# Kernel optimization log

Measured on AMD Instinct MI355X. Metric: run time of the kernel, lower is better.

## Reference

```python
import jax, jax.numpy as jnp
import numpy as np

B, S, D, H, L, FF = 1, 2048, 512, 8, 4, 2048
DH = D // H


def _sincos(n, d):
    theta = 1.0 / (10000.0 ** (np.arange(0, d, 2, dtype=np.float64) / d))
    ang = np.arange(n, dtype=np.float64)[:, None] * theta[None, :]
    sin = np.repeat(np.sin(ang), 2, axis=-1).astype(np.float32)
    cos = np.repeat(np.cos(ang), 2, axis=-1).astype(np.float32)
    return jnp.asarray(sin), jnp.asarray(cos)  # [n, d]


def _rot(x):
    # rotate pairs: (x1, x2) -> (-x2, x1), interleaved
    x1, x2 = x[..., 0::2], x[..., 1::2]
    return jnp.stack([-x2, x1], axis=-1).reshape(x.shape)


def _theta_shift(x, sin, cos):
    return x * cos + _rot(x) * sin


def _decay_mask(n, h):
    # RetNet per-head decay gammas: 1 - exp(linspace(log(1/32), log(1/512), h))
    gammas = 1.0 - np.exp(np.linspace(np.log(1.0 / 32.0), np.log(1.0 / 512.0), h))
    dist = np.arange(n)[:, None] - np.arange(n)[None, :]
    m = np.where(dist >= 0, gammas[:, None, None] ** np.maximum(dist, 0), 0.0)
    return jnp.asarray(m, dtype=jnp.float32)  # [h, n, n]


def _ln(x, w, b, eps=1e-5):
    mu = x.mean(-1, keepdims=True)
    var = ((x - mu) ** 2).mean(-1, keepdims=True)
    return (x - mu) * jax.lax.rsqrt(var + eps) * w + b


def setup_inputs() -> dict:
    key = jax.random.key(0)
    ks = jax.random.split(key, 12)
    sc = 0.02
    nrm = lambda k, shp: jax.random.normal(k, shp, jnp.float32) * sc
    return {
        "x": jax.random.normal(ks[0], (B, S, D), jnp.float32),
        "pos_emb": nrm(ks[1], (5000, D)),
        "Wq": nrm(ks[2], (L, D, D)), "bq": jnp.zeros((L, D), jnp.float32),
        "Wk": nrm(ks[3], (L, D, D)), "bk": jnp.zeros((L, D), jnp.float32),
        "Wv": nrm(ks[4], (L, D, D)), "bv": jnp.zeros((L, D), jnp.float32),
        "Wg": nrm(ks[5], (L, D, D)), "bg": jnp.zeros((L, D), jnp.float32),
        "Wo": nrm(ks[6], (L, D, D)), "bo": jnp.zeros((L, D), jnp.float32),
        "ln1w": jnp.ones((L, D), jnp.float32), "ln1b": jnp.zeros((L, D), jnp.float32),
        "ln2w": jnp.ones((L, D), jnp.float32), "ln2b": jnp.zeros((L, D), jnp.float32),
        "W1": nrm(ks[7], (L, D, FF)), "b1": jnp.zeros((L, FF), jnp.float32),
        "W2": nrm(ks[8], (L, FF, D)), "b2": jnp.zeros((L, D), jnp.float32),
        "Wout": nrm(ks[9], (D, 1)), "bout": jnp.zeros((1,), jnp.float32),
    }


def reference(x, pos_emb, Wq, bq, Wk, bk, Wv, bv, Wg, bg, Wo, bo,
              ln1w, ln1b, ln2w, ln2b, W1, b1, W2, b2, Wout, bout):
    b, s, d = x.shape
    # faithful to source: pos_emb[:x.shape[0]] (requires B==1 to broadcast)
    x = x + pos_emb[: x.shape[0]]
    sin, cos = _sincos(s, DH)
    dmask = _decay_mask(s, H)  # [h, s, s]
    inv_scale = 1.0 / jnp.sqrt(jnp.float32(DH))

    def heads(t):  # [b,s,d] -> [b,h,s,dh]
        return t.reshape(b, s, H, DH).transpose(0, 2, 1, 3)

    for l in range(L):
        # --- multi-scale retention block (pre-LN) ---
        y = _ln(x, ln1w[l], ln1b[l])
        q = heads(y @ Wq[l] + bq[l])
        k = heads(y @ Wk[l] + bk[l])
        v = heads(y @ Wv[l] + bv[l])
        q = _theta_shift(q, sin, cos) * inv_scale
        k = _theta_shift(k, sin, cos)
        sim = jnp.einsum("bhnd,bhmd->bhnm", q, k) * dmask  # decay-masked QK^T
        ret = jnp.einsum("bhnm,bhmd->bhnd", sim, v)
        # per-head group norm (no affine)
        mu = ret.mean(-1, keepdims=True)
        var = ((ret - mu) ** 2).mean(-1, keepdims=True)
        ret = (ret - mu) * jax.lax.rsqrt(var + 1e-6)
        ret = ret.transpose(0, 2, 1, 3).reshape(b, s, d)
        g = jax.nn.silu(y @ Wg[l] + bg[l])
        x = x + (g * ret) @ Wo[l] + bo[l]
        # --- FFN block (pre-LN, swish) ---
        z = _ln(x, ln2w[l], ln2b[l])
        x = x + jax.nn.silu(z @ W1[l] + b1[l]) @ W2[l] + b2[l]

    return jax.nn.sigmoid(x @ Wout + bout)  # [b, s, 1]
```

## Files before the change

kernel.cpp:

```cpp
#include <hip/hip_runtime.h>
#include <math.h>
#include <stdint.h>

#define SEQ 2048
#define DMODEL 512
#define NH 8
#define DHEAD 64
#define NL 4
#define DFF 2048

typedef __attribute__((ext_vector_type(8))) short short8;
typedef __attribute__((ext_vector_type(4))) float f32x4;

__device__ __forceinline__ short f2bf(float f) {
  unsigned u = __float_as_uint(f);
  u += 0x7fffu + ((u >> 16) & 1u);
  return (short)(u >> 16);
}
__device__ __forceinline__ float silu_f(float x) { return x / (1.f + __expf(-x)); }

__device__ __forceinline__ void cp16(const void* g, void* l) {
  __builtin_amdgcn_global_load_lds(
      (const __attribute__((address_space(1))) unsigned*)(unsigned long long)(uintptr_t)g,
      (__attribute__((address_space(3))) unsigned*)(unsigned)(uintptr_t)l, 16, 0, 0);
}

__global__ __launch_bounds__(256) void k_transpose(const float* __restrict__ src, short* __restrict__ dst,
                                                   int rows, int cols) {
  __shared__ float tile[32][33];
  size_t zoff = (size_t)blockIdx.z * rows * cols;
  src += zoff; dst += zoff;
  int bx = blockIdx.x * 32, by = blockIdx.y * 32;
  int tx = threadIdx.x & 31, ty = threadIdx.x >> 5;
#pragma unroll
  for (int k = 0; k < 4; ++k)
    tile[ty + k * 8][tx] = src[(size_t)(by + ty + k * 8) * cols + bx + tx];
  __syncthreads();
#pragma unroll
  for (int k = 0; k < 4; ++k)
    dst[(size_t)(bx + ty + k * 8) * rows + by + tx] = f2bf(tile[tx][ty + k * 8]);
}

__global__ void k_addpos(const float* __restrict__ xi, const float* __restrict__ pos, float* __restrict__ xo) {
  int i = blockIdx.x * 256 + threadIdx.x;
  float4 a = ((const float4*)xi)[i];
  float4 p = ((const float4*)pos)[i & 127];
  a.x += p.x; a.y += p.y; a.z += p.z; a.w += p.w;
  ((float4*)xo)[i] = a;
}

__global__ void k_sincos(float* __restrict__ sn, float* __restrict__ cs) {
  int g = blockIdx.x * 256 + threadIdx.x;
  int s = g >> 5, p = g & 31;
  double inv = pow(10000.0, -(double)p / 32.0);
  double a = (double)s * inv;
  float sv = (float)sin(a), cv = (float)cos(a);
  sn[s * DHEAD + 2 * p] = sv; sn[s * DHEAD + 2 * p + 1] = sv;
  cs[s * DHEAD + 2 * p] = cv; cs[s * DHEAD + 2 * p + 1] = cv;
}

__global__ __launch_bounds__(256) void k_ln(const float* __restrict__ x, const float* __restrict__ w,
                                            const float* __restrict__ b, short* __restrict__ o, float eps) {
  int wid = threadIdx.x >> 6, lane = threadIdx.x & 63;
  int row = blockIdx.x * 4 + wid;
  const float* xr = x + (size_t)row * DMODEL;
  float4 v0 = *(const float4*)(xr + lane * 8);
  float4 v1 = *(const float4*)(xr + lane * 8 + 4);
  float sm = v0.x + v0.y + v0.z + v0.w + v1.x + v1.y + v1.z + v1.w;
  float sq = v0.x * v0.x + v0.y * v0.y + v0.z * v0.z + v0.w * v0.w +
             v1.x * v1.x + v1.y * v1.y + v1.z * v1.z + v1.w * v1.w;
#pragma unroll
  for (int m = 1; m < 64; m <<= 1) { sm += __shfl_xor(sm, m); sq += __shfl_xor(sq, m); }
  float mu = sm * (1.f / 512.f);
  float rstd = rsqrtf(sq * (1.f / 512.f) - mu * mu + eps);
  const float* wr = w + lane * 8; const float* br = b + lane * 8;
  float vals[8] = {v0.x, v0.y, v0.z, v0.w, v1.x, v1.y, v1.z, v1.w};
  short t[8] __attribute__((aligned(16)));
#pragma unroll
  for (int i = 0; i < 8; ++i) t[i] = f2bf((vals[i] - mu) * rstd * wr[i] + br[i]);
  *(int4*)(o + (size_t)row * DMODEL + lane * 8) = *(int4*)t;
}

struct GB { const short* A; const short* Bt; const float* bias; void* out; int mode; };
struct GArgs { GB b[4]; int M, N, K; };

__global__ __launch_bounds__(256) void k_gemm(GArgs ga) {
  const GB g = ga.b[blockIdx.z];
  const int K = ga.K, N = ga.N, M = ga.M;
  const int n0 = blockIdx.x * 64;
  const int m0 = blockIdx.y * 64;
  const int tid = threadIdx.x;
  const int w = tid >> 6, lane = tid & 63, l16 = lane & 15, quad = lane >> 4;
  const int wm = (w & 1) * 32, wn = (w >> 1) * 32;
  __shared__ __align__(16) short As[2][4096];
  __shared__ __align__(16) short Bs[2][4096];

  const short* Ab = g.A + (size_t)m0 * K;
  const short* Bb = g.Bt + (size_t)n0 * K;
  const int rsub = lane >> 3;
  const int cch = (lane & 7) ^ rsub;
  const int nIter = K >> 6;

  auto stage = [&](int buf, int k0) {
#pragma unroll
    for (int c = 0; c < 2; ++c) {
      int seg = w + 4 * c;
      cp16(Ab + (size_t)(seg * 8 + rsub) * K + k0 + cch * 8, &As[buf][seg * 512]);
      cp16(Bb + (size_t)(seg * 8 + rsub) * K + k0 + cch * 8, &Bs[buf][seg * 512]);
    }
  };

  f32x4 acc[2][2];
#pragma unroll
  for (int a = 0; a < 2; ++a)
#pragma unroll
    for (int b = 0; b < 2; ++b) acc[a][b] = {0.f, 0.f, 0.f, 0.f};

  stage(0, 0);
  for (int it = 0; it < nIter; ++it) {
    __syncthreads();
    if (it + 1 < nIter) stage((it + 1) & 1, (it + 1) << 6);
    const short* as = As[it & 1];
    const short* bs = Bs[it & 1];
#pragma unroll
    for (int kki = 0; kki < 2; ++kki) {
      int ch = ((quad + 4 * kki) ^ (l16 & 7)) * 8;
      short8 af[2], bfv[2];
#pragma unroll
      for (int a = 0; a < 2; ++a) af[a] = *(const short8*)&as[(wm + a * 16 + l16) * 64 + ch];
#pragma unroll
      for (int b = 0; b < 2; ++b) bfv[b] = *(const short8*)&bs[(wn + b * 16 + l16) * 64 + ch];
#pragma unroll
      for (int a = 0; a < 2; ++a)
#pragma unroll
        for (int b = 0; b < 2; ++b)
          acc[a][b] = __builtin_amdgcn_mfma_f32_16x16x32_bf16(af[a], bfv[b], acc[a][b], 0, 0, 0);
    }
  }
#pragma unroll
  for (int a = 0; a < 2; ++a) {
#pragma unroll
    for (int b = 0; b < 2; ++b) {
      int row0 = m0 + wm + a * 16 + quad * 4;
      int col = n0 + wn + b * 16 + l16;
      float vals[4];
#pragma unroll
      for (int r = 0; r < 4; ++r) vals[r] = acc[a][b][r] + g.bias[col];
      if (g.mode == 4) {
        short t4[4] __attribute__((aligned(8)));
#pragma unroll
        for (int r = 0; r < 4; ++r) t4[r] = f2bf(vals[r]);
        *(uint2*)&((short*)g.out)[(size_t)col * M + row0] = *(const uint2*)t4;
      } else if (g.mode == 0) {
#pragma unroll
        for (int r = 0; r < 4; ++r) ((float*)g.out)[(size_t)(row0 + r) * N + col] = vals[r];
      } else if (g.mode == 1) {
#pragma unroll
        for (int r = 0; r < 4; ++r) ((short*)g.out)[(size_t)(row0 + r) * N + col] = f2bf(silu_f(vals[r]));
      } else {
#pragma unroll
        for (int r = 0; r < 4; ++r) ((float*)g.out)[(size_t)(row0 + r) * N + col] += vals[r];
      }
    }
  }
}

__global__ __launch_bounds__(256) void k_rope(const float* __restrict__ q, const float* __restrict__ k,
                                              const float* __restrict__ sn, const float* __restrict__ cs,
                                              short* __restrict__ qo, short* __restrict__ ko) {
  int s = blockIdx.x * 2 + (threadIdx.x >> 7);
  int idx = (threadIdx.x & 127) * 4;
  int d = idx & 63;
  size_t base = (size_t)s * DMODEL + idx;
  float4 qv = *(const float4*)(q + base);
  float4 kv = *(const float4*)(k + base);
  float4 sv = *(const float4*)(sn + s * DHEAD + d);
  float4 cv = *(const float4*)(cs + s * DHEAD + d);
  short qt[4] __attribute__((aligned(8))), kt[4] __attribute__((aligned(8)));
  qt[0] = f2bf((qv.x * cv.x - qv.y * sv.x) * 0.125f);
  qt[1] = f2bf((qv.y * cv.y + qv.x * sv.y) * 0.125f);
  qt[2] = f2bf((qv.z * cv.z - qv.w * sv.z) * 0.125f);
  qt[3] = f2bf((qv.w * cv.w + qv.z * sv.w) * 0.125f);
  kt[0] = f2bf(kv.x * cv.x - kv.y * sv.x);
  kt[1] = f2bf(kv.y * cv.y + kv.x * sv.y);
  kt[2] = f2bf(kv.z * cv.z - kv.w * sv.z);
  kt[3] = f2bf(kv.w * cv.w + kv.z * sv.w);
  *(uint2*)(qo + base) = *(const uint2*)qt;
  *(uint2*)(ko + base) = *(const uint2*)kt;
}

__global__ __launch_bounds__(256) void k_attn(const short* __restrict__ qb, const short* __restrict__ kb,
                                              const short* __restrict__ vtb, float* __restrict__ r0,
                                              float* __restrict__ r1) {
  int x = blockIdx.x, hd = blockIdx.y, jc = blockIdx.z;
  int ib = jc ? (31 - x) : x;
  int t = threadIdx.x;
  int w = t >> 6, lane = t & 63, l16 = lane & 15, quad = lane >> 4;
  __shared__ __align__(16) short smem[4 * 64 * 72];
  short* qs = smem;
  short* kt = smem + 4608;
  short* vt = smem + 9216;
  short* p  = smem + 13824;

  double stepd = (log(1.0 / 512.0) - log(1.0 / 32.0)) / 7.0;
  double gam = 1.0 - exp(log(1.0 / 32.0) + hd * stepd);
  float l2g = (float)(log(gam) * 1.4426950408889634);

  for (int c = t; c < 512; c += 256) {
    int r = c >> 3, d8 = (c & 7) * 8;
    *(short8*)&qs[r * 72 + d8] = *(const short8*)&qb[(size_t)(ib * 64 + r) * DMODEL + hd * DHEAD + d8];
  }
  f32x4 oacc[4];
#pragma unroll
  for (int b = 0; b < 4; ++b) oacc[b] = {0.f, 0.f, 0.f, 0.f};

  for (int jb = jc; jb <= ib; jb += 2) {
    __syncthreads();
    for (int c = t; c < 512; c += 256) {
      int r = c >> 3, d8 = (c & 7) * 8;
      *(short8*)&kt[r * 72 + d8] = *(const short8*)&kb[(size_t)(jb * 64 + r) * DMODEL + hd * DHEAD + d8];
      *(short8*)&vt[r * 72 + d8] = *(const short8*)&vtb[(size_t)(hd * DHEAD + r) * SEQ + jb * 64 + d8];
    }
    __syncthreads();
    f32x4 sacc[4];
#pragma unroll
    for (int b = 0; b < 4; ++b) sacc[b] = {0.f, 0.f, 0.f, 0.f};
#pragma unroll
    for (int kk = 0; kk < 64; kk += 32) {
      short8 af = *(const short8*)&qs[(w * 16 + l16) * 72 + kk + quad * 8];
#pragma unroll
      for (int b = 0; b < 4; ++b) {
        short8 bf_ = *(const short8*)&kt[(b * 16 + l16) * 72 + kk + quad * 8];
        sacc[b] = __builtin_amdgcn_mfma_f32_16x16x32_bf16(af, bf_, sacc[b], 0, 0, 0);
      }
    }
    int dtile = (ib - jb) * 64;
#pragma unroll
    for (int b = 0; b < 4; ++b) {
#pragma unroll
      for (int r = 0; r < 4; ++r) {
        int iloc = w * 16 + quad * 4 + r;
        int jloc = b * 16 + l16;
        int df = dtile + iloc - jloc;
        float dec = (df < 0) ? 0.f : exp2f(l2g * (float)df);
        p[iloc * 72 + jloc] = f2bf(sacc[b][r] * dec);
      }
    }
    __syncthreads();
#pragma unroll
    for (int kk = 0; kk < 64; kk += 32) {
      short8 af = *(const short8*)&vt[(w * 16 + l16) * 72 + kk + quad * 8];
#pragma unroll
      for (int b = 0; b < 4; ++b) {
        short8 bf_ = *(const short8*)&p[(b * 16 + l16) * 72 + kk + quad * 8];
        oacc[b] = __builtin_amdgcn_mfma_f32_16x16x32_bf16(af, bf_, oacc[b], 0, 0, 0);
      }
    }
  }
  __syncthreads();
  float* obuf = (float*)smem;
#pragma unroll
  for (int b = 0; b < 4; ++b) {
#pragma unroll
    for (int r = 0; r < 4; ++r) {
      int d = w * 16 + quad * 4 + r;
      int i = b * 16 + l16;
      obuf[i * 68 + d] = oacc[b][r];
    }
  }
  __syncthreads();
  float* rp = jc ? r1 : r0;
  for (int c = t; c < 1024; c += 256) {
    int r = c >> 4, d4 = (c & 15) * 4;
    *(float4*)&rp[(size_t)(ib * 64 + r) * DMODEL + hd * DHEAD + d4] = *(const float4*)&obuf[r * 68 + d4];
  }
}

__global__ __launch_bounds__(256) void k_retgate(const float* __restrict__ r0, const float* __restrict__ r1,
                                                 const float* __restrict__ g, short* __restrict__ o) {
  int wid = threadIdx.x >> 6, lane = threadIdx.x & 63;
  int row = blockIdx.x * 4 + wid;
  int s = row >> 3, hd = row & 7;
  size_t base = (size_t)s * DMODEL + hd * DHEAD + lane;
  float v = r0[base] + r1[base];
  float sm = v, sq = v * v;
#pragma unroll
  for (int m = 1; m < 64; m <<= 1) { sm += __shfl_xor(sm, m); sq += __shfl_xor(sq, m); }
  float mu = sm * (1.f / 64.f);
  float var = sq * (1.f / 64.f) - mu * mu;
  float rn = (v - mu) * rsqrtf(var + 1e-6f);
  o[base] = f2bf(silu_f(g[base]) * rn);
}

__global__ __launch_bounds__(256) void k_final(const float* __restrict__ x, const float* __restrict__ w,
                                               const float* __restrict__ bo, float* __restrict__ o) {
  int wid = threadIdx.x >> 6, lane = threadIdx.x & 63;
  int row = blockIdx.x * 4 + wid;
  const float* xr = x + (size_t)row * DMODEL;
  float4 a0 = *(const float4*)(xr + lane * 8), a1 = *(const float4*)(xr + lane * 8 + 4);
  float4 w0 = *(const float4*)(w + lane * 8), w1 = *(const float4*)(w + lane * 8 + 4);
  float sm = a0.x * w0.x + a0.y * w0.y + a0.z * w0.z + a0.w * w0.w +
             a1.x * w1.x + a1.y * w1.y + a1.z * w1.z + a1.w * w1.w;
#pragma unroll
  for (int m = 1; m < 64; m <<= 1) sm += __shfl_xor(sm, m);
  if (lane == 0) o[row] = 1.f / (1.f + __expf(-(sm + bo[0])));
}

extern "C" void kernel_launch(void* const* d_in, const int* in_sizes, int n_in,
                              void* d_out, int out_size, void* d_ws, size_t ws_size,
                              hipStream_t stream) {
  const float* x_in = (const float*)d_in[0];
  const float* pos = (const float*)d_in[1];
  const float* Wq = (const float*)d_in[2];  const float* bq = (const float*)d_in[3];
  const float* Wk = (const float*)d_in[4];  const float* bk = (const float*)d_in[5];
  const float* Wv = (const float*)d_in[6];  const float* bv = (const float*)d_in[7];
  const float* Wg = (const float*)d_in[8];  const float* bg = (const float*)d_in[9];
  const float* Wo = (const float*)d_in[10]; const float* bo = (const float*)d_in[11];
  const float* ln1w = (const float*)d_in[12]; const float* ln1b = (const float*)d_in[13];
  const float* ln2w = (const float*)d_in[14]; const float* ln2b = (const float*)d_in[15];
  const float* W1 = (const float*)d_in[16]; const float* b1 = (const float*)d_in[17];
  const float* W2 = (const float*)d_in[18]; const float* b2 = (const float*)d_in[19];
  const float* Wout = (const float*)d_in[20]; const float* bout = (const float*)d_in[21];
  float* out = (float*)d_out;

  char* ws = (char*)d_ws;
  size_t off = 0;
  auto alloc = [&](size_t bytes) -> void* {
    void* p = ws + off;
    off += (bytes + 255) & ~(size_t)255;
    return p;
  };
  const size_t DD = (size_t)DMODEL * DMODEL;
  short* wqt = (short*)alloc((size_t)NL * DD * 2);
  short* wkt = (short*)alloc((size_t)NL * DD * 2);
  short* wvt = (short*)alloc((size_t)NL * DD * 2);
  short* wgt = (short*)alloc((size_t)NL * DD * 2);
  short* wot = (short*)alloc((size_t)NL * DD * 2);
  short* w1t = (short*)alloc((size_t)NL * DMODEL * DFF * 2);
  short* w2t = (short*)alloc((size_t)NL * DMODEL * DFF * 2);
  float* xb = (float*)alloc((size_t)SEQ * DMODEL * 4);
  short* ybf = (short*)alloc((size_t)SEQ * DMODEL * 2);
  float* qraw = (float*)alloc((size_t)SEQ * DMODEL * 4);
  float* kraw = (float*)alloc((size_t)SEQ * DMODEL * 4);
  float* graw = (float*)alloc((size_t)SEQ * DMODEL * 4);
  short* qb = (short*)alloc((size_t)SEQ * DMODEL * 2);
  short* kb = (short*)alloc((size_t)SEQ * DMODEL * 2);
  short* vtb = (short*)alloc((size_t)SEQ * DMODEL * 2);
  float* ret0 = (float*)alloc((size_t)SEQ * DMODEL * 4);
  float* ret1 = (float*)alloc((size_t)SEQ * DMODEL * 4);
  short* grb = (short*)alloc((size_t)SEQ * DMODEL * 2);
  short* zbf = (short*)alloc((size_t)SEQ * DMODEL * 2);
  short* hbf = (short*)alloc((size_t)SEQ * DFF * 2);
  float* sint = (float*)alloc((size_t)SEQ * DHEAD * 4);
  float* cost = (float*)alloc((size_t)SEQ * DHEAD * 4);

  k_transpose<<<dim3(DMODEL / 32, DMODEL / 32, NL), 256, 0, stream>>>(Wq, wqt, DMODEL, DMODEL);
  k_transpose<<<dim3(DMODEL / 32, DMODEL / 32, NL), 256, 0, stream>>>(Wk, wkt, DMODEL, DMODEL);
  k_transpose<<<dim3(DMODEL / 32, DMODEL / 32, NL), 256, 0, stream>>>(Wv, wvt, DMODEL, DMODEL);
  k_transpose<<<dim3(DMODEL / 32, DMODEL / 32, NL), 256, 0, stream>>>(Wg, wgt, DMODEL, DMODEL);
  k_transpose<<<dim3(DMODEL / 32, DMODEL / 32, NL), 256, 0, stream>>>(Wo, wot, DMODEL, DMODEL);
  k_transpose<<<dim3(DFF / 32, DMODEL / 32, NL), 256, 0, stream>>>(W1, w1t, DMODEL, DFF);
  k_transpose<<<dim3(DMODEL / 32, DFF / 32, NL), 256, 0, stream>>>(W2, w2t, DFF, DMODEL);
  k_addpos<<<SEQ * DMODEL / 1024, 256, 0, stream>>>(x_in, pos, xb);
  k_sincos<<<SEQ * 32 / 256, 256, 0, stream>>>(sint, cost);

  for (int l = 0; l < NL; ++l) {
    k_ln<<<SEQ / 4, 256, 0, stream>>>(xb, ln1w + l * DMODEL, ln1b + l * DMODEL, ybf, 1e-5f);
    GArgs gq{};
    gq.M = SEQ; gq.N = DMODEL; gq.K = DMODEL;
    gq.b[0] = GB{ybf, wqt + l * DD, bq + l * DMODEL, qraw, 0};
    gq.b[1] = GB{ybf, wkt + l * DD, bk + l * DMODEL, kraw, 0};
    gq.b[2] = GB{ybf, wvt + l * DD, bv + l * DMODEL, vtb, 4};
    gq.b[3] = GB{ybf, wgt + l * DD, bg + l * DMODEL, graw, 0};
    k_gemm<<<dim3(DMODEL / 64, SEQ / 64, 4), 256, 0, stream>>>(gq);
    k_rope<<<SEQ / 2, 256, 0, stream>>>(qraw, kraw, sint, cost, qb, kb);
    k_attn<<<dim3(32, NH, 2), 256, 0, stream>>>(qb, kb, vtb, ret0, ret1);
    k_retgate<<<SEQ * NH / 4, 256, 0, stream>>>(ret0, ret1, graw, grb);
    GArgs go{};
    go.M = SEQ; go.N = DMODEL; go.K = DMODEL;
    go.b[0] = GB{grb, wot + l * DD, bo + l * DMODEL, xb, 2};
    k_gemm<<<dim3(DMODEL / 64, SEQ / 64, 1), 256, 0, stream>>>(go);
    k_ln<<<SEQ / 4, 256, 0, stream>>>(xb, ln2w + l * DMODEL, ln2b + l * DMODEL, zbf, 1e-5f);
    GArgs g1{};
    g1.M = SEQ; g1.N = DFF; g1.K = DMODEL;
    g1.b[0] = GB{zbf, w1t + (size_t)l * DMODEL * DFF, b1 + l * DFF, hbf, 1};
    k_gemm<<<dim3(DFF / 64, SEQ / 64, 1), 256, 0, stream>>>(g1);
    GArgs g2{};
    g2.M = SEQ; g2.N = DMODEL; g2.K = DFF;
    g2.b[0] = GB{hbf, w2t + (size_t)l * DMODEL * DFF, b2 + l * DMODEL, xb, 2};
    k_gemm<<<dim3(DMODEL / 64, SEQ / 64, 1), 256, 0, stream>>>(g2);
  }
  k_final<<<SEQ / 4, 256, 0, stream>>>(xb, Wout, bout, out);
}
```

Baseline: 561.1 us.

## Fuse layernorm, rope, retention-gate into GEMM prologues/epilogues; split-K with atomics

Folds the pre-LN into the A-operand load of the QKVG and FFN1 GEMMs, folds rope and scaling into the Q/K GEMM epilogue, and folds the retention group-norm and SiLU gate into the Wo GEMM prologue. The Wo and FFN2 GEMMs now use a two-way split-K that accumulates into the residual with atomicAdd, and the weight transposes and init kernels are merged into single launches. This removes several launches and the intermediate float and bf16 buffer round-trips through memory. In exchange, the LN prologue recomputes row statistics in every N-tile block, and the split-K atomics make the summation order nondeterministic.

```diff
diff --git a/kernel.cpp b/kernel.cpp
--- a/kernel.cpp
+++ b/kernel.cpp
@@ -25,88 +25,83 @@
       (__attribute__((address_space(3))) unsigned*)(unsigned)(uintptr_t)l, 16, 0, 0);
 }
 
-__global__ __launch_bounds__(256) void k_transpose(const float* __restrict__ src, short* __restrict__ dst,
-                                                   int rows, int cols) {
+struct TP { const float* src; short* dst; int rows, cols, base; };
+struct TPs { TP t[7]; };
+__global__ __launch_bounds__(256) void k_prep(TPs ts) {
+  int bid = blockIdx.x;
+  int di = 6;
+  while (di > 0 && bid < ts.t[di].base) --di;
+  TP d = ts.t[di];
+  int local = bid - d.base;
+  int tx = d.cols >> 5, ty = d.rows >> 5;
+  int tpz = tx * ty;
+  int z = local / tpz, rem = local - z * tpz;
+  int bx = (rem % tx) * 32, by = (rem / tx) * 32;
+  const float* src = d.src + (size_t)z * d.rows * d.cols;
+  short* dst = d.dst + (size_t)z * d.rows * d.cols;
   __shared__ float tile[32][33];
-  size_t zoff = (size_t)blockIdx.z * rows * cols;
-  src += zoff; dst += zoff;
-  int bx = blockIdx.x * 32, by = blockIdx.y * 32;
-  int tx = threadIdx.x & 31, ty = threadIdx.x >> 5;
+  int txi = threadIdx.x & 31, tyi = threadIdx.x >> 5;
 #pragma unroll
   for (int k = 0; k < 4; ++k)
-    tile[ty + k * 8][tx] = src[(size_t)(by + ty + k * 8) * cols + bx + tx];
+    tile[tyi + k * 8][txi] = src[(size_t)(by + tyi + k * 8) * d.cols + bx + txi];
   __syncthreads();
 #pragma unroll
   for (int k = 0; k < 4; ++k)
-    dst[(size_t)(bx + ty + k * 8) * rows + by + tx] = f2bf(tile[tx][ty + k * 8]);
-}
-
-__global__ void k_addpos(const float* __restrict__ xi, const float* __restrict__ pos, float* __restrict__ xo) {
-  int i = blockIdx.x * 256 + threadIdx.x;
-  float4 a = ((const float4*)xi)[i];
-  float4 p = ((const float4*)pos)[i & 127];
-  a.x += p.x; a.y += p.y; a.z += p.z; a.w += p.w;
-  ((float4*)xo)[i] = a;
-}
-
-__global__ void k_sincos(float* __restrict__ sn, float* __restrict__ cs) {
-  int g = blockIdx.x * 256 + threadIdx.x;
-  int s = g >> 5, p = g & 31;
-  double inv = pow(10000.0, -(double)p / 32.0);
-  double a = (double)s * inv;
-  float sv = (float)sin(a), cv = (float)cos(a);
-  sn[s * DHEAD + 2 * p] = sv; sn[s * DHEAD + 2 * p + 1] = sv;
-  cs[s * DHEAD + 2 * p] = cv; cs[s * DHEAD + 2 * p + 1] = cv;
-}
-
-__global__ __launch_bounds__(256) void k_ln(const float* __restrict__ x, const float* __restrict__ w,
-                                            const float* __restrict__ b, short* __restrict__ o, float eps) {
-  int wid = threadIdx.x >> 6, lane = threadIdx.x & 63;
-  int row = blockIdx.x * 4 + wid;
-  const float* xr = x + (size_t)row * DMODEL;
-  float4 v0 = *(const float4*)(xr + lane * 8);
-  float4 v1 = *(const float4*)(xr + lane * 8 + 4);
-  float sm = v0.x + v0.y + v0.z + v0.w + v1.x + v1.y + v1.z + v1.w;
-  float sq = v0.x * v0.x + v0.y * v0.y + v0.z * v0.z + v0.w * v0.w +
-             v1.x * v1.x + v1.y * v1.y + v1.z * v1.z + v1.w * v1.w;
-#pragma unroll
-  for (int m = 1; m < 64; m <<= 1) { sm += __shfl_xor(sm, m); sq += __shfl_xor(sq, m); }
-  float mu = sm * (1.f / 512.f);
-  float rstd = rsqrtf(sq * (1.f / 512.f) - mu * mu + eps);
-  const float* wr = w + lane * 8; const float* br = b + lane * 8;
-  float vals[8] = {v0.x, v0.y, v0.z, v0.w, v1.x, v1.y, v1.z, v1.w};
-  short t[8] __attribute__((aligned(16)));
-#pragma unroll
-  for (int i = 0; i < 8; ++i) t[i] = f2bf((vals[i] - mu) * rstd * wr[i] + br[i]);
-  *(int4*)(o + (size_t)row * DMODEL + lane * 8) = *(int4*)t;
-}
-
-struct GB { const short* A; const short* Bt; const float* bias; void* out; int mode; };
-struct GArgs { GB b[4]; int M, N, K; };
-
-__global__ __launch_bounds__(256) void k_gemm(GArgs ga) {
-  const GB g = ga.b[blockIdx.z];
+    dst[(size_t)(bx + tyi + k * 8) * d.rows + by + txi] = f2bf(tile[txi][tyi + k * 8]);
+}
+
+__global__ void k_init(const float* __restrict__ xi, const float* __restrict__ pos, float* __restrict__ xo,
+                       float* __restrict__ sn, float* __restrict__ cs) {
+  if (blockIdx.x < 1024) {
+    int i = blockIdx.x * 256 + threadIdx.x;
+    float4 a = ((const float4*)xi)[i];
+    float4 p = ((const float4*)pos)[i & 127];
+    a.x += p.x; a.y += p.y; a.z += p.z; a.w += p.w;
+    ((float4*)xo)[i] = a;
+  } else {
+    int g = (blockIdx.x - 1024) * 256 + threadIdx.x;
+    int s = g >> 5, p = g & 31;
+    double inv = pow(10000.0, -(double)p / 32.0);
+    double a = (double)s * inv;
+    float sv = (float)sin(a), cv = (float)cos(a);
+    sn[s * DHEAD + 2 * p] = sv; sn[s * DHEAD + 2 * p + 1] = sv;
+    cs[s * DHEAD + 2 * p] = cv; cs[s * DHEAD + 2 * p + 1] = cv;
+  }
+}
+
+struct GB { const short* Bt; const float* bias; void* out; int mode; };
+struct GP {
+  const void* A; const float* A2; const float* A3;
+  const float* lnw; const float* lnb;
+  const float* sn; const float* cs;
+  GB b[4];
+  int M, N, K, kspl;
+};
+
+template <int APRO>
+__global__ __launch_bounds__(256) void k_gemm(GP ga) {
+  const int z = blockIdx.z;
+  GB gb; int k0, klen;
+  if (ga.kspl > 0) { gb = ga.b[0]; k0 = z * ga.kspl; klen = ga.kspl; }
+  else { gb = ga.b[z]; k0 = 0; klen = ga.K; }
   const int K = ga.K, N = ga.N, M = ga.M;
-  const int n0 = blockIdx.x * 64;
-  const int m0 = blockIdx.y * 64;
+  const int n0 = blockIdx.x * 64, m0 = blockIdx.y * 64;
   const int tid = threadIdx.x;
   const int w = tid >> 6, lane = tid & 63, l16 = lane & 15, quad = lane >> 4;
   const int wm = (w & 1) * 32, wn = (w >> 1) * 32;
-  __shared__ __align__(16) short As[2][4096];
+  const int nIter = klen >> 6;
+
   __shared__ __align__(16) short Bs[2][4096];
-
-  const short* Ab = g.A + (size_t)m0 * K;
-  const short* Bb = g.Bt + (size_t)n0 * K;
-  const int rsub = lane >> 3;
-  const int cch = (lane & 7) ^ rsub;
-  const int nIter = K >> 6;
-
-  auto stage = [&](int buf, int k0) {
+  __shared__ __align__(16) short As[APRO == 0 ? 8192 : 4608];
+  __shared__ float fext[APRO == 2 ? 512 : 128];
+
+  const int rsub = lane >> 3, cch = (lane & 7) ^ rsub;
+  const short* Bb = gb.Bt + (size_t)n0 * K + k0;
+  auto stageB = [&](int buf, int it) {
 #pragma unroll
     for (int c = 0; c < 2; ++c) {
       int seg = w + 4 * c;
-      cp16(Ab + (size_t)(seg * 8 + rsub) * K + k0 + cch * 8, &As[buf][seg * 512]);
-      cp16(Bb + (size_t)(seg * 8 + rsub) * K + k0 + cch * 8, &Bs[buf][seg * 512]);
+      cp16(Bb + (size_t)(seg * 8 + rsub) * K + (it << 6) + cch * 8, &Bs[buf][seg * 512]);
     }
   };
 
@@ -116,77 +111,200 @@
 #pragma unroll
     for (int b = 0; b < 2; ++b) acc[a][b] = {0.f, 0.f, 0.f, 0.f};
 
-  stage(0, 0);
-  for (int it = 0; it < nIter; ++it) {
+  if constexpr (APRO == 0) {
+    const short* Ab = (const short*)ga.A + (size_t)m0 * K + k0;
+    auto stageA = [&](int buf, int it) {
+#pragma unroll
+      for (int c = 0; c < 2; ++c) {
+        int seg = w + 4 * c;
+        cp16(Ab + (size_t)(seg * 8 + rsub) * K + (it << 6) + cch * 8, &As[buf * 4096 + seg * 512]);
+      }
+    };
+    stageA(0, 0); stageB(0, 0);
+    for (int it = 0; it < nIter; ++it) {
+      __syncthreads();
+      if (it + 1 < nIter) { stageA((it + 1) & 1, it + 1); stageB((it + 1) & 1, it + 1); }
+      const short* as = &As[(it & 1) * 4096];
+      const short* bs = Bs[it & 1];
+#pragma unroll
+      for (int kki = 0; kki < 2; ++kki) {
+        int ch = ((quad + 4 * kki) ^ (l16 & 7)) * 8;
+        short8 af[2], bfv[2];
+#pragma unroll
+        for (int a = 0; a < 2; ++a) af[a] = *(const short8*)&as[(wm + a * 16 + l16) * 64 + ch];
+#pragma unroll
+        for (int b = 0; b < 2; ++b) bfv[b] = *(const short8*)&bs[(wn + b * 16 + l16) * 64 + ch];
+#pragma unroll
+        for (int a = 0; a < 2; ++a)
+#pragma unroll
+          for (int b = 0; b < 2; ++b)
+            acc[a][b] = __builtin_amdgcn_mfma_f32_16x16x32_bf16(af[a], bfv[b], acc[a][b], 0, 0, 0);
+      }
+    }
+  } else if constexpr (APRO == 1) {
+    const float* X = (const float*)ga.A;
+    stageB(0, 0);
+    for (int i = 0; i < 16; ++i) {
+      int row = w * 16 + i;
+      const float* xr = X + (size_t)(m0 + row) * K;
+      float4 v0 = *(const float4*)(xr + lane * 8);
+      float4 v1 = *(const float4*)(xr + lane * 8 + 4);
+      float sm = v0.x + v0.y + v0.z + v0.w + v1.x + v1.y + v1.z + v1.w;
+      float sq = v0.x * v0.x + v0.y * v0.y + v0.z * v0.z + v0.w * v0.w +
+                 v1.x * v1.x + v1.y * v1.y + v1.z * v1.z + v1.w * v1.w;
+#pragma unroll
+      for (int m = 1; m < 64; m <<= 1) { sm += __shfl_xor(sm, m); sq += __shfl_xor(sq, m); }
+      float mu = sm * (1.f / 512.f);
+      float rstd = rsqrtf(sq * (1.f / 512.f) - mu * mu + 1e-5f);
+      if (lane == 0) { fext[row * 2] = mu; fext[row * 2 + 1] = rstd; }
+    }
+    const int arow = tid >> 2, ac2 = (tid & 3) * 2;
+    const float* Arow = X + (size_t)(m0 + arow) * K;
+    float4 xa[4], lw[4], lb[4];
+    auto loadA = [&](int it) {
+      int kk = k0 + (it << 6) + ac2 * 8;
+      xa[0] = *(const float4*)(Arow + kk);     xa[1] = *(const float4*)(Arow + kk + 4);
+      xa[2] = *(const float4*)(Arow + kk + 8); xa[3] = *(const float4*)(Arow + kk + 12);
+      lw[0] = *(const float4*)(ga.lnw + kk);     lw[1] = *(const float4*)(ga.lnw + kk + 4);
+      lw[2] = *(const float4*)(ga.lnw + kk + 8); lw[3] = *(const float4*)(ga.lnw + kk + 12);
+      lb[0] = *(const float4*)(ga.lnb + kk);     lb[1] = *(const float4*)(ga.lnb + kk + 4);
+      lb[2] = *(const float4*)(ga.lnb + kk + 8); lb[3] = *(const float4*)(ga.lnb + kk + 12);
+    };
+    loadA(0);
     __syncthreads();
-    if (it + 1 < nIter) stage((it + 1) & 1, (it + 1) << 6);
-    const short* as = As[it & 1];
-    const short* bs = Bs[it & 1];
-#pragma unroll
-    for (int kki = 0; kki < 2; ++kki) {
-      int ch = ((quad + 4 * kki) ^ (l16 & 7)) * 8;
-      short8 af[2], bfv[2];
-#pragma unroll
-      for (int a = 0; a < 2; ++a) af[a] = *(const short8*)&as[(wm + a * 16 + l16) * 64 + ch];
-#pragma unroll
-      for (int b = 0; b < 2; ++b) bfv[b] = *(const short8*)&bs[(wn + b * 16 + l16) * 64 + ch];
-#pragma unroll
-      for (int a = 0; a < 2; ++a)
-#pragma unroll
-        for (int b = 0; b < 2; ++b)
-          acc[a][b] = __builtin_amdgcn_mfma_f32_16x16x32_bf16(af[a], bfv[b], acc[a][b], 0, 0, 0);
-    }
-  }
+    const float mu = fext[arow * 2], rstd = fext[arow * 2 + 1];
+    for (int it = 0; it < nIter; ++it) {
+      short sh[16] __attribute__((aligned(16)));
+#pragma unroll
+      for (int j = 0; j < 4; ++j) {
+        sh[j * 4 + 0] = f2bf((xa[j].x - mu) * rstd * lw[j].x + lb[j].x);
+        sh[j * 4 + 1] = f2bf((xa[j].y - mu) * rstd * lw[j].y + lb[j].y);
+        sh[j * 4 + 2] = f2bf((xa[j].z - mu) * rstd * lw[j].z + lb[j].z);
+        sh[j * 4 + 3] = f2bf((xa[j].w - mu) * rstd * lw[j].w + lb[j].w);
+      }
+      *(short8*)&As[arow * 72 + ac2 * 8] = *(short8*)&sh[0];
+      *(short8*)&As[arow * 72 + ac2 * 8 + 8] = *(short8*)&sh[8];
+      __syncthreads();
+      if (it + 1 < nIter) { stageB((it + 1) & 1, it + 1); loadA(it + 1); }
+      const short* bs = Bs[it & 1];
+#pragma unroll
+      for (int kki = 0; kki < 2; ++kki) {
+        int chb = ((quad + 4 * kki) ^ (l16 & 7)) * 8;
+        short8 af[2], bfv[2];
+#pragma unroll
+        for (int a = 0; a < 2; ++a) af[a] = *(const short8*)&As[(wm + a * 16 + l16) * 72 + kki * 32 + quad * 8];
+#pragma unroll
+        for (int b = 0; b < 2; ++b) bfv[b] = *(const short8*)&bs[(wn + b * 16 + l16) * 64 + chb];
+#pragma unroll
+        for (int a = 0; a < 2; ++a)
+#pragma unroll
+          for (int b = 0; b < 2; ++b)
+            acc[a][b] = __builtin_amdgcn_mfma_f32_16x16x32_bf16(af[a], bfv[b], acc[a][b], 0, 0, 0);
+      }
+      __syncthreads();
+    }
+  } else {
+    const float* R0 = (const float*)ga.A;
+    const float* R1 = ga.A2;
+    const float* Gg = ga.A3;
+    const int arow = tid >> 2, ac2 = (tid & 3) * 2;
+    const size_t rbase = (size_t)(m0 + arow) * K;
+    stageB(0, 0);
+    for (int it = 0; it < nIter; ++it) {
+      int kk = k0 + (it << 6) + ac2 * 8;
+      float4 v[4];
+#pragma unroll
+      for (int j = 0; j < 4; ++j) {
+        float4 a0 = *(const float4*)(R0 + rbase + kk + j * 4);
+        float4 a1 = *(const float4*)(R1 + rbase + kk + j * 4);
+        v[j].x = a0.x + a1.x; v[j].y = a0.y + a1.y; v[j].z = a0.z + a1.z; v[j].w = a0.w + a1.w;
+      }
+      float ps = 0.f, psq = 0.f;
+#pragma unroll
+      for (int j = 0; j < 4; ++j) {
+        ps += v[j].x + v[j].y + v[j].z + v[j].w;
+        psq += v[j].x * v[j].x + v[j].y * v[j].y + v[j].z * v[j].z + v[j].w * v[j].w;
+      }
+      fext[arow * 8 + (tid & 3) * 2] = ps;
+      fext[arow * 8 + (tid & 3) * 2 + 1] = psq;
+      __syncthreads();
+      float sm = 0.f, sq = 0.f;
+#pragma unroll
+      for (int j = 0; j < 4; ++j) { sm += fext[arow * 8 + j * 2]; sq += fext[arow * 8 + j * 2 + 1]; }
+      float mu = sm * (1.f / 64.f);
+      float rstd = rsqrtf(sq * (1.f / 64.f) - mu * mu + 1e-6f);
+      short sh[16] __attribute__((aligned(16)));
+#pragma unroll
+      for (int j = 0; j < 4; ++j) {
+        float4 gv = *(const float4*)(Gg + rbase + kk + j * 4);
+        sh[j * 4 + 0] = f2bf((v[j].x - mu) * rstd * silu_f(gv.x));
+        sh[j * 4 + 1] = f2bf((v[j].y - mu) * rstd * silu_f(gv.y));
+        sh[j * 4 + 2] = f2bf((v[j].z - mu) * rstd * silu_f(gv.z));
+        sh[j * 4 + 3] = f2bf((v[j].w - mu) * rstd * silu_f(gv.w));
+      }
+      *(short8*)&As[arow * 72 + ac2 * 8] = *(short8*)&sh[0];
+      *(short8*)&As[arow * 72 + ac2 * 8 + 8] = *(short8*)&sh[8];
+      __syncthreads();
+      if (it + 1 < nIter) stageB((it + 1) & 1, it + 1);
+      const short* bs = Bs[it & 1];
+#pragma unroll
+      for (int kki = 0; kki < 2; ++kki) {
+        int chb = ((quad + 4 * kki) ^ (l16 & 7)) * 8;
+        short8 af[2], bfv[2];
+#pragma unroll
+        for (int a = 0; a < 2; ++a) af[a] = *(const short8*)&As[(wm + a * 16 + l16) * 72 + kki * 32 + quad * 8];
+#pragma unroll
+        for (int b = 0; b < 2; ++b) bfv[b] = *(const short8*)&bs[(wn + b * 16 + l16) * 64 + chb];
+#pragma unroll
+        for (int a = 0; a < 2; ++a)
+#pragma unroll
+          for (int b = 0; b < 2; ++b)
+            acc[a][b] = __builtin_amdgcn_mfma_f32_16x16x32_bf16(af[a], bfv[b], acc[a][b], 0, 0, 0);
+      }
+      __syncthreads();
+    }
+  }
+
+  const int mode = gb.mode;
 #pragma unroll
   for (int a = 0; a < 2; ++a) {
 #pragma unroll
     for (int b = 0; b < 2; ++b) {
       int row0 = m0 + wm + a * 16 + quad * 4;
       int col = n0 + wn + b * 16 + l16;
+      float bi = (mode == 2 && k0 > 0) ? 0.f : gb.bias[col];
       float vals[4];
 #pragma unroll
-      for (int r = 0; r < 4; ++r) vals[r] = acc[a][b][r] + g.bias[col];
-      if (g.mode == 4) {
+      for (int r = 0; r < 4; ++r) vals[r] = acc[a][b][r] + bi;
+      if (mode == 5 || mode == 6) {
+        float sc = (mode == 5) ? 0.125f : 1.f;
+        int d = col & 63;
+#pragma unroll
+        for (int r = 0; r < 4; ++r) {
+          int s = row0 + r;
+          float vv = vals[r];
+          float p = __shfl_xor(vv, 1);
+          float rot = (col & 1) ? p : -p;
+          float o = (vv * ga.cs[s * 64 + d] + rot * ga.sn[s * 64 + d]) * sc;
+          ((short*)gb.out)[(size_t)s * DMODEL + col] = f2bf(o);
+        }
+      } else if (mode == 4) {
         short t4[4] __attribute__((aligned(8)));
 #pragma unroll
         for (int r = 0; r < 4; ++r) t4[r] = f2bf(vals[r]);
-        *(uint2*)&((short*)g.out)[(size_t)col * M + row0] = *(const uint2*)t4;
-      } else if (g.mode == 0) {
-#pragma unroll
-        for (int r = 0; r < 4; ++r) ((float*)g.out)[(size_t)(row0 + r) * N + col] = vals[r];
-      } else if (g.mode == 1) {
-#pragma unroll
-        for (int r = 0; r < 4; ++r) ((short*)g.out)[(size_t)(row0 + r) * N + col] = f2bf(silu_f(vals[r]));
+        *(uint2*)&((short*)gb.out)[(size_t)col * M + row0] = *(const uint2*)t4;
+      } else if (mode == 0) {
+#pragma unroll
+        for (int r = 0; r < 4; ++r) ((float*)gb.out)[(size_t)(row0 + r) * N + col] = vals[r];
+      } else if (mode == 1) {
+#pragma unroll
+        for (int r = 0; r < 4; ++r) ((short*)gb.out)[(size_t)(row0 + r) * N + col] = f2bf(silu_f(vals[r]));
       } else {
 #pragma unroll
-        for (int r = 0; r < 4; ++r) ((float*)g.out)[(size_t)(row0 + r) * N + col] += vals[r];
-      }
-    }
-  }
-}
-
-__global__ __launch_bounds__(256) void k_rope(const float* __restrict__ q, const float* __restrict__ k,
-                                              const float* __restrict__ sn, const float* __restrict__ cs,
-                                              short* __restrict__ qo, short* __restrict__ ko) {
-  int s = blockIdx.x * 2 + (threadIdx.x >> 7);
-  int idx = (threadIdx.x & 127) * 4;
-  int d = idx & 63;
-  size_t base = (size_t)s * DMODEL + idx;
-  float4 qv = *(const float4*)(q + base);
-  float4 kv = *(const float4*)(k + base);
-  float4 sv = *(const float4*)(sn + s * DHEAD + d);
-  float4 cv = *(const float4*)(cs + s * DHEAD + d);
-  short qt[4] __attribute__((aligned(8))), kt[4] __attribute__((aligned(8)));
-  qt[0] = f2bf((qv.x * cv.x - qv.y * sv.x) * 0.125f);
-  qt[1] = f2bf((qv.y * cv.y + qv.x * sv.y) * 0.125f);
-  qt[2] = f2bf((qv.z * cv.z - qv.w * sv.z) * 0.125f);
-  qt[3] = f2bf((qv.w * cv.w + qv.z * sv.w) * 0.125f);
-  kt[0] = f2bf(kv.x * cv.x - kv.y * sv.x);
-  kt[1] = f2bf(kv.y * cv.y + kv.x * sv.y);
-  kt[2] = f2bf(kv.z * cv.z - kv.w * sv.z);
-  kt[3] = f2bf(kv.w * cv.w + kv.z * sv.w);
-  *(uint2*)(qo + base) = *(const uint2*)qt;
-  *(uint2*)(ko + base) = *(const uint2*)kt;
+        for (int r = 0; r < 4; ++r) atomicAdd(&((float*)gb.out)[(size_t)(row0 + r) * N + col], vals[r]);
+      }
+    }
+  }
 }
 
 __global__ __launch_bounds__(256) void k_attn(const short* __restrict__ qb, const short* __restrict__ kb,
@@ -274,22 +392,6 @@
     int r = c >> 4, d4 = (c & 15) * 4;
     *(float4*)&rp[(size_t)(ib * 64 + r) * DMODEL + hd * DHEAD + d4] = *(const float4*)&obuf[r * 68 + d4];
   }
-}
-
-__global__ __launch_bounds__(256) void k_retgate(const float* __restrict__ r0, const float* __restrict__ r1,
-                                                 const float* __restrict__ g, short* __restrict__ o) {
-  int wid = threadIdx.x >> 6, lane = threadIdx.x & 63;
-  int row = blockIdx.x * 4 + wid;
-  int s = row >> 3, hd = row & 7;
-  size_t base = (size_t)s * DMODEL + hd * DHEAD + lane;
-  float v = r0[base] + r1[base];
-  float sm = v, sq = v * v;
-#pragma unroll
-  for (int m = 1; m < 64; m <<= 1) { sm += __shfl_xor(sm, m); sq += __shfl_xor(sq, m); }
-  float mu = sm * (1.f / 64.f);
-  float var = sq * (1.f / 64.f) - mu * mu;
-  float rn = (v - mu) * rsqrtf(var + 1e-6f);
-  o[base] = f2bf(silu_f(g[base]) * rn);
 }
 
 __global__ __launch_bounds__(256) void k_final(const float* __restrict__ x, const float* __restrict__ w,
@@ -339,56 +441,57 @@
   short* w1t = (short*)alloc((size_t)NL * DMODEL * DFF * 2);
   short* w2t = (short*)alloc((size_t)NL * DMODEL * DFF * 2);
   float* xb = (float*)alloc((size_t)SEQ * DMODEL * 4);
-  short* ybf = (short*)alloc((size_t)SEQ * DMODEL * 2);
-  float* qraw = (float*)alloc((size_t)SEQ * DMODEL * 4);
-  float* kraw = (float*)alloc((size_t)SEQ * DMODEL * 4);
   float* graw = (float*)alloc((size_t)SEQ * DMODEL * 4);
   short* qb = (short*)alloc((size_t)SEQ * DMODEL * 2);
   short* kb = (short*)alloc((size_t)SEQ * DMODEL * 2);
   short* vtb = (short*)alloc((size_t)SEQ * DMODEL * 2);
   float* ret0 = (float*)alloc((size_t)SEQ * DMODEL * 4);
   float* ret1 = (float*)alloc((size_t)SEQ * DMODEL * 4);
-  short* grb = (short*)alloc((size_t)SEQ * DMODEL * 2);
-  short* zbf = (short*)alloc((size_t)SEQ * DMODEL * 2);
   short* hbf = (short*)alloc((size_t)SEQ * DFF * 2);
   float* sint = (float*)alloc((size_t)SEQ * DHEAD * 4);
   float* cost = (float*)alloc((size_t)SEQ * DHEAD * 4);
 
-  k_transpose<<<dim3(DMODEL / 32, DMODEL / 32, NL), 256, 0, stream>>>(Wq, wqt, DMODEL, DMODEL);
-  k_transpose<<<dim3(DMODEL / 32, DMODEL / 32, NL), 256, 0, stream>>>(Wk, wkt, DMODEL, DMODEL);
-  k_transpose<<<dim3(DMODEL / 32, DMODEL / 32, NL), 256, 0, stream>>>(Wv, wvt, DMODEL, DMODEL);
-  k_transpose<<<dim3(DMODEL / 32, DMODEL / 32, NL), 256, 0, stream>>>(Wg, wgt, DMODEL, DMODEL);
-  k_transpose<<<dim3(DMODEL / 32, DMODEL / 32, NL), 256, 0, stream>>>(Wo, wot, DMODEL, DMODEL);
-  k_transpose<<<dim3(DFF / 32, DMODEL / 32, NL), 256, 0, stream>>>(W1, w1t, DMODEL, DFF);
-  k_transpose<<<dim3(DMODEL / 32, DFF / 32, NL), 256, 0, stream>>>(W2, w2t, DFF, DMODEL);
-  k_addpos<<<SEQ * DMODEL / 1024, 256, 0, stream>>>(x_in, pos, xb);
-  k_sincos<<<SEQ * 32 / 256, 256, 0, stream>>>(sint, cost);
+  TPs tp;
+  tp.t[0] = TP{Wq, wqt, DMODEL, DMODEL, 0};
+  tp.t[1] = TP{Wk, wkt, DMODEL, DMODEL, 1024};
+  tp.t[2] = TP{Wv, wvt, DMODEL, DMODEL, 2048};
+  tp.t[3] = TP{Wg, wgt, DMODEL, DMODEL, 3072};
+  tp.t[4] = TP{Wo, wot, DMODEL, DMODEL, 4096};
+  tp.t[5] = TP{W1, w1t, DMODEL, DFF, 5120};
+  tp.t[6] = TP{W2, w2t, DFF, DMODEL, 9216};
+  k_prep<<<13312, 256, 0, stream>>>(tp);
+  k_init<<<1280, 256, 0, stream>>>(x_in, pos, xb, sint, cost);
 
   for (int l = 0; l < NL; ++l) {
-    k_ln<<<SEQ / 4, 256, 0, stream>>>(xb, ln1w + l * DMODEL, ln1b + l * DMODEL, ybf, 1e-5f);
-    GArgs gq{};
-    gq.M = SEQ; gq.N = DMODEL; gq.K = DMODEL;
-    gq.b[0] = GB{ybf, wqt + l * DD, bq + l * DMODEL, qraw, 0};
-    gq.b[1] = GB{ybf, wkt + l * DD, bk + l * DMODEL, kraw, 0};
-    gq.b[2] = GB{ybf, wvt + l * DD, bv + l * DMODEL, vtb, 4};
-    gq.b[3] = GB{ybf, wgt + l * DD, bg + l * DMODEL, graw, 0};
-    k_gemm<<<dim3(DMODEL / 64, SEQ / 64, 4), 256, 0, stream>>>(gq);
-    k_rope<<<SEQ / 2, 256, 0, stream>>>(qraw, kraw, sint, cost, qb, kb);
+    GP gq{};
+    gq.A = xb; gq.lnw = ln1w + l * DMODEL; gq.lnb = ln1b + l * DMODEL;
+    gq.sn = sint; gq.cs = cost;
+    gq.b[0] = GB{wqt + l * DD, bq + l * DMODEL, qb, 5};
+    gq.b[1] = GB{wkt + l * DD, bk + l * DMODEL, kb, 6};
+    gq.b[2] = GB{wvt + l * DD, bv + l * DMODEL, vtb, 4};
+    gq.b[3] = GB{wgt + l * DD, bg + l * DMODEL, graw, 0};
+    gq.M = SEQ; gq.N = DMODEL; gq.K = DMODEL; gq.kspl = 0;
+    k_gemm<1><<<dim3(8, 32, 4), 256, 0, stream>>>(gq);
+
     k_attn<<<dim3(32, NH, 2), 256, 0, stream>>>(qb, kb, vtb, ret0, ret1);
-    k_retgate<<<SEQ * NH / 4, 256, 0, stream>>>(ret0, ret1, graw, grb);
-    GArgs go{};
-    go.M = SEQ; go.N = DMODEL; go.K = DMODEL;
-    go.b[0] = GB{grb, wot + l * DD, bo + l * DMODEL, xb, 2};
-    k_gemm<<<dim3(DMODEL / 64, SEQ / 64, 1), 256, 0, stream>>>(go);
-    k_ln<<<SEQ / 4, 256, 0, stream>>>(xb, ln2w + l * DMODEL, ln2b + l * DMODEL, zbf, 1e-5f);
-    GArgs g1{};
-    g1.M = SEQ; g1.N = DFF; g1.K = DMODEL;
-    g1.b[0] = GB{zbf, w1t + (size_t)l * DMODEL * DFF, b1 + l * DFF, hbf, 1};
-    k_gemm<<<dim3(DFF / 64, SEQ / 64, 1), 256, 0, stream>>>(g1);
-    GArgs g2{};
-    g2.M = SEQ; g2.N = DMODEL; g2.K = DFF;
-    g2.b[0] = GB{hbf, w2t + (size_t)l * DMODEL * DFF, b2 + l * DMODEL, xb, 2};
-    k_gemm<<<dim3(DMODEL / 64, SEQ / 64, 1), 256, 0, stream>>>(g2);
+
+    GP gw{};
+    gw.A = ret0; gw.A2 = ret1; gw.A3 = graw;
+    gw.b[0] = GB{wot + l * DD, bo + l * DMODEL, xb, 2};
+    gw.M = SEQ; gw.N = DMODEL; gw.K = DMODEL; gw.kspl = 256;
+    k_gemm<2><<<dim3(8, 32, 2), 256, 0, stream>>>(gw);
+
+    GP g1{};
+    g1.A = xb; g1.lnw = ln2w + l * DMODEL; g1.lnb = ln2b + l * DMODEL;
+    g1.b[0] = GB{w1t + (size_t)l * DMODEL * DFF, b1 + l * DFF, hbf, 1};
+    g1.M = SEQ; g1.N = DFF; g1.K = DMODEL; g1.kspl = 0;
+    k_gemm<1><<<dim3(32, 32, 1), 256, 0, stream>>>(g1);
+
+    GP g2{};
+    g2.A = hbf;
+    g2.b[0] = GB{w2t + (size_t)l * DMODEL * DFF, b2 + l * DMODEL, xb, 2};
+    g2.M = SEQ; g2.N = DMODEL; g2.K = DFF; g2.kspl = 1024;
+    k_gemm<0><<<dim3(8, 32, 2), 256, 0, stream>>>(g2);
   }
   k_final<<<SEQ / 4, 256, 0, stream>>>(xb, Wout, bout, out);
 }
```

After: 767.7 us. 36.8% more time.
